# Kernel tuning notes

Hardware: AMD Instinct MI355X
Metric: run time of the kernel (lower is better)

## Reference

```python
import jax, jax.numpy as jnp
import numpy as np

NUM_HEADS = 16
HEAD_DIM = 80
DIM = NUM_HEADS * HEAD_DIM
SEQ = 2048
SCALE = HEAD_DIM ** -0.5


def rotate_half(x):
    x1, x2 = jnp.split(x, 2, axis=-1)
    return jnp.concatenate((-x2, x1), axis=-1)


def setup_inputs() -> dict:
    key = jax.random.key(0)
    ks = jax.random.split(key, 8)
    hidden_states = jax.random.normal(ks[0], (SEQ, DIM), dtype=jnp.float32)
    cu_seqlens = jnp.array([0, SEQ], dtype=jnp.int32)  # unused by the math
    # rotary embeddings for head_dim
    inv_freq = 1.0 / (10000.0 ** (jnp.arange(0, HEAD_DIM // 2, dtype=jnp.float32) / (HEAD_DIM // 2)))
    freqs = jnp.outer(jnp.arange(SEQ, dtype=jnp.float32), inv_freq)  # [S, hd/2]
    emb = jnp.concatenate((freqs, freqs), axis=-1)  # [S, hd]
    cos = jnp.cos(emb)
    sin = jnp.sin(emb)
    w_qkv = jax.random.normal(ks[1], (3 * DIM, DIM), dtype=jnp.float32) * (DIM ** -0.5)
    b_qkv = jax.random.normal(ks[2], (3 * DIM,), dtype=jnp.float32) * 0.02
    w_proj = jax.random.normal(ks[3], (DIM, DIM), dtype=jnp.float32) * (DIM ** -0.5)
    b_proj = jax.random.normal(ks[4], (DIM,), dtype=jnp.float32) * 0.02
    return {"hidden_states": hidden_states, "cu_seqlens": cu_seqlens, "cos": cos,
            "sin": sin, "w_qkv": w_qkv, "b_qkv": b_qkv, "w_proj": w_proj, "b_proj": b_proj}


def reference(hidden_states, cu_seqlens, cos, sin, w_qkv, b_qkv, w_proj, b_proj):
    S = hidden_states.shape[0]
    qkv = hidden_states @ w_qkv.T + b_qkv  # [S, 3*D]
    qkv = qkv.reshape(S, 3, NUM_HEADS, HEAD_DIM)
    q, k, v = qkv[:, 0], qkv[:, 1], qkv[:, 2]  # each [S, H, hd]
    c = cos[:, None, :]  # [S, 1, hd]
    s = sin[:, None, :]
    q = q * c + rotate_half(q) * s
    k = k * c + rotate_half(k) * s
    # SDPA, non-causal: [H, S, S]
    scores = jnp.einsum('shd,thd->hst', q, k) * SCALE
    attn = jax.nn.softmax(scores, axis=-1)
    out = jnp.einsum('hst,thd->shd', attn, v).reshape(S, DIM)
    return out @ w_proj.T + b_proj
```

## Files before the change

### kernel.cpp

```cpp
#include <hip/hip_runtime.h>


#define SEQLEN   2048
#define DIMM     1280
#define NHEADS   16
#define HD       80
#define HDP      96
#define QKV_N    3840
#define NSPLIT   4
#define KVSPAN   (SEQLEN / NSPLIT)
#define QSCALE_LOG2E 0.16130083587064776f

#define KSTRIDE  104
#define VSTRIDE  72
#define PSTRIDE  72

#define EXP2F(x) __builtin_amdgcn_exp2f(x)

#define GLD16(gptr, lptr)                                                      \
    __builtin_amdgcn_global_load_lds(                                          \
        (const __attribute__((address_space(1))) void*)(gptr),                 \
        (__attribute__((address_space(3))) void*)(lptr), 16, 0, 0)

typedef float f32x4 __attribute__((ext_vector_type(4)));
typedef _Float16 half8 __attribute__((ext_vector_type(8)));
typedef _Float16 half4 __attribute__((ext_vector_type(4)));

static __device__ __forceinline__ f32x4 mfma_16x16x32(half8 a, half8 b, f32x4 c) {
    return __builtin_amdgcn_mfma_f32_16x16x32_f16(a, b, c, 0, 0, 0);
}

__global__ void cast_f32_f16(const float* __restrict__ src,
                             _Float16* __restrict__ dst, int n4) {
    int i = blockIdx.x * blockDim.x + threadIdx.x;
    if (i < n4) {
        const float4 v = ((const float4*)src)[i];
        half4 h;
        h.x = (_Float16)v.x; h.y = (_Float16)v.y;
        h.z = (_Float16)v.z; h.w = (_Float16)v.w;
        ((half4*)dst)[i] = h;
    }
}

template<bool OUT_F16>
__global__ __launch_bounds__(256, 2)
void gemm_bt(const _Float16* __restrict__ A, const _Float16* __restrict__ B,
             const float* __restrict__ bias, void* __restrict__ Cout,
             int M, int N, int K) {
    __shared__ __align__(16) _Float16 As[128 * 32];
    __shared__ __align__(16) _Float16 Bs[128 * 32];
    const int tid  = threadIdx.x;
    const int lane = tid & 63;
    const int wave = tid >> 6;
    const int l15  = lane & 15;
    const int quad = lane >> 4;
    const int wm   = wave & 1;
    const int wn   = wave >> 1;
    const long bm = blockIdx.x, bn = blockIdx.y;

    const _Float16* Ag = A + bm * 128 * (long)K;
    const _Float16* Bg = B + bn * 128 * (long)K;

    const int srow = lane >> 2;
    const int scol = (lane & 3) * 8;
    f32x4 acc[4][4] = {};

    for (int k0 = 0; k0 < K; k0 += 32) {
        __syncthreads();
#pragma unroll
        for (int cc = 0; cc < 2; cc++) {
            const int c = wave + cc * 4;
            const long row = 16 * c + srow;
            GLD16(Ag + row * K + k0 + scol, As + 512 * c + lane * 8);
            GLD16(Bg + row * K + k0 + scol, Bs + 512 * c + lane * 8);
        }
        __syncthreads();
        half8 af[4], bf[4];
#pragma unroll
        for (int t = 0; t < 4; t++) {
            af[t] = *(const half8*)&As[(wm * 64 + t * 16 + l15) * 32 + quad * 8];
            bf[t] = *(const half8*)&Bs[(wn * 64 + t * 16 + l15) * 32 + quad * 8];
        }
#pragma unroll
        for (int mt = 0; mt < 4; mt++)
#pragma unroll
            for (int nt = 0; nt < 4; nt++)
                acc[mt][nt] = mfma_16x16x32(af[mt], bf[nt], acc[mt][nt]);
    }

    float bv[4];
#pragma unroll
    for (int nt = 0; nt < 4; nt++)
        bv[nt] = bias[bn * 128 + wn * 64 + nt * 16 + l15];

#pragma unroll
    for (int mt = 0; mt < 4; mt++) {
#pragma unroll
        for (int r = 0; r < 4; r++) {
            const long row = bm * 128 + wm * 64 + mt * 16 + quad * 4 + r;
#pragma unroll
            for (int nt = 0; nt < 4; nt++) {
                const long col = bn * 128 + wn * 64 + nt * 16 + l15;
                const float v = acc[mt][nt][r] + bv[nt];
                if (OUT_F16) ((_Float16*)Cout)[row * (long)N + col] = (_Float16)v;
                else         ((float*)Cout)[row * (long)N + col] = v;
            }
        }
    }
}

__global__ void rope_repack(const _Float16* __restrict__ qkv,
                            const float* __restrict__ cosb,
                            const float* __restrict__ sinb,
                            _Float16* __restrict__ Qh,
                            _Float16* __restrict__ Kh,
                            _Float16* __restrict__ Vh) {
    const int s = blockIdx.x;
    const int tid = threadIdx.x;
    const _Float16* row = qkv + (long)s * QKV_N;

    for (int i = tid; i < NHEADS * 40; i += 256) {
        const int h = i / 40, d = i - h * 40;
        const float c  = cosb[s * HD + d];
        const float sn = sinb[s * HD + d];
        const long o = ((long)h * SEQLEN + s) * HDP;
        const float q0 = (float)row[h * HD + d];
        const float q1 = (float)row[h * HD + d + 40];
        Qh[o + d]      = (_Float16)((q0 * c - q1 * sn) * QSCALE_LOG2E);
        Qh[o + d + 40] = (_Float16)((q1 * c + q0 * sn) * QSCALE_LOG2E);
        const float k0 = (float)row[DIMM + h * HD + d];
        const float k1 = (float)row[DIMM + h * HD + d + 40];
        Kh[o + d]      = (_Float16)(k0 * c - k1 * sn);
        Kh[o + d + 40] = (_Float16)(k1 * c + k0 * sn);
    }
    for (int i = tid; i < NHEADS * HD; i += 256) {
        const int h = i / HD, d = i - h * HD;
        Vh[((long)h * SEQLEN + s) * HDP + d] = row[2 * DIMM + i];
    }
    for (int i = tid; i < NHEADS * 16; i += 256) {
        const int h = i >> 4, d = HD + (i & 15);
        const long o = ((long)h * SEQLEN + s) * HDP + d;
        Qh[o] = (_Float16)0.f; Kh[o] = (_Float16)0.f;
    }
}

__global__ __launch_bounds__(256)
void v_transpose(const _Float16* __restrict__ Vh, _Float16* __restrict__ Vt) {
    const int s0 = blockIdx.x * 64;
    const int h  = blockIdx.y;
    __shared__ __align__(16) _Float16 Ts[64 * 88];
    const int tid = threadIdx.x;
    for (int i = tid; i < 640; i += 256) {
        const int r = i / 10, c = (i - r * 10) * 8;
        *(half8*)&Ts[r * 88 + c] =
            *(const half8*)&Vh[((long)h * SEQLEN + s0 + r) * HDP + c];
    }
    __syncthreads();
    for (int i = tid; i < 640; i += 256) {
        const int d = i >> 3, sc = (i & 7) * 8;
        half8 v;
#pragma unroll
        for (int j = 0; j < 8; j++) v[j] = Ts[(sc + j) * 88 + d];
        *(half8*)&Vt[((long)h * HD + d) * SEQLEN + s0 + sc] = v;
    }
}

__global__ __launch_bounds__(512, 6)
void attn_kernel(const _Float16* __restrict__ Qh, const _Float16* __restrict__ Kh,
                 const _Float16* __restrict__ Vt,
                 _Float16* __restrict__ Ohat0, _Float16* __restrict__ Ohat1,
                 float* __restrict__ Lpart) {
    const int s0 = blockIdx.x * 128;
    const int h  = blockIdx.y;
    const int z  = blockIdx.z;
    __shared__ __align__(16) _Float16 Ks[64 * KSTRIDE];
    __shared__ __align__(16) _Float16 Vts[HD * VSTRIDE];
    __shared__ __align__(16) _Float16 Ps[8][16 * PSTRIDE];

    const int tid  = threadIdx.x;
    const int lane = tid & 63;
    const int wave = tid >> 6;
    const int l15  = lane & 15;
    const int quad = lane >> 4;

    const _Float16* Qg = Qh + ((long)h * SEQLEN + s0 + wave * 16 + l15) * HDP;
    half8 qf[3];
#pragma unroll
    for (int kk = 0; kk < 3; kk++)
        qf[kk] = *(const half8*)&Qg[kk * 32 + quad * 8];

    f32x4 oacc[5] = {};
    float l_r[4] = {0.f, 0.f, 0.f, 0.f};

    for (int t0 = z * KVSPAN; t0 < (z + 1) * KVSPAN; t0 += 64) {
        __syncthreads();
        const _Float16* Kg = Kh + ((long)h * SEQLEN + t0) * HDP;
        for (int i = tid; i < 768; i += 512) {
            const int r = i / 12, c = (i - r * 12) * 8;
            *(half8*)&Ks[r * KSTRIDE + c] = *(const half8*)&Kg[(long)r * HDP + c];
        }
        const _Float16* Vtg = Vt + (long)h * HD * SEQLEN + t0;
        for (int i = tid; i < 640; i += 512) {
            const int d = i >> 3, c = (i & 7) * 8;
            *(half8*)&Vts[d * VSTRIDE + c] = *(const half8*)&Vtg[(long)d * SEQLEN + c];
        }
        __syncthreads();

        f32x4 sa[4] = {};
#pragma unroll
        for (int kk = 0; kk < 3; kk++)
#pragma unroll
            for (int ct = 0; ct < 4; ct++) {
                half8 b = *(const half8*)&Ks[(ct * 16 + l15) * KSTRIDE + kk * 32 + quad * 8];
                sa[ct] = mfma_16x16x32(qf[kk], b, sa[ct]);
            }

        float p[4][4];
#pragma unroll
        for (int ct = 0; ct < 4; ct++)
#pragma unroll
            for (int r = 0; r < 4; r++) {
                p[ct][r] = EXP2F(sa[ct][r]);
                l_r[r] += p[ct][r];
                Ps[wave][(quad * 4 + r) * PSTRIDE + ct * 16 + l15] = (_Float16)p[ct][r];
            }
        asm volatile("s_waitcnt lgkmcnt(0)" ::: "memory");
        half8 pf0 = *(const half8*)&Ps[wave][l15 * PSTRIDE + quad * 8];
        half8 pf1 = *(const half8*)&Ps[wave][l15 * PSTRIDE + 32 + quad * 8];
#pragma unroll
        for (int nt = 0; nt < 5; nt++) {
            half8 v0 = *(const half8*)&Vts[(nt * 16 + l15) * VSTRIDE + quad * 8];
            half8 v1 = *(const half8*)&Vts[(nt * 16 + l15) * VSTRIDE + 32 + quad * 8];
            oacc[nt] = mfma_16x16x32(pf0, v0, oacc[nt]);
            oacc[nt] = mfma_16x16x32(pf1, v1, oacc[nt]);
        }
    }

#pragma unroll
    for (int off = 1; off < 16; off <<= 1)
#pragma unroll
        for (int r = 0; r < 4; r++)
            l_r[r] += __shfl_xor(l_r[r], off);

    float inv[4];
#pragma unroll
    for (int r = 0; r < 4; r++) inv[r] = 1.0f / l_r[r];

    _Float16* Oz = (z < 2) ? Ohat0 : Ohat1;
    const long obase = ((long)(z & 1) * NHEADS + h) * SEQLEN;
    const long lbase = ((long)z * NHEADS + h) * SEQLEN;
#pragma unroll
    for (int nt = 0; nt < 5; nt++)
#pragma unroll
        for (int r = 0; r < 4; r++) {
            const long row = s0 + wave * 16 + quad * 4 + r;
            Oz[(obase + row) * HD + nt * 16 + l15] = (_Float16)(oacc[nt][r] * inv[r]);
        }
    if (l15 == 0)
#pragma unroll
        for (int r = 0; r < 4; r++)
            Lpart[lbase + s0 + wave * 16 + quad * 4 + r] = l_r[r];
}

__global__ __launch_bounds__(256)
void attn_combine(const _Float16* __restrict__ Ohat0,
                  const _Float16* __restrict__ Ohat1,
                  const float* __restrict__ Lp,
                  _Float16* __restrict__ attnb) {
    const int i = blockIdx.x * 256 + threadIdx.x;
    if (i >= SEQLEN * DIMM / 4) return;
    const int flat = i * 4;
    const int s = flat / DIMM;
    const int rem = flat - s * DIMM;
    const int h = rem / HD;
    const int d = rem - h * HD;
    float l[NSPLIT], lsum = 0.f;
#pragma unroll
    for (int zi = 0; zi < NSPLIT; zi++) {
        l[zi] = Lp[((long)zi * NHEADS + h) * SEQLEN + s];
        lsum += l[zi];
    }
    const float invl = 1.0f / lsum;
    float acc[4] = {0.f, 0.f, 0.f, 0.f};
#pragma unroll
    for (int zi = 0; zi < NSPLIT; zi++) {
        const _Float16* Oz = (zi < 2) ? Ohat0 : Ohat1;
        const long obase = ((long)(zi & 1) * NHEADS + h) * SEQLEN;
        const half4 o = *(const half4*)&Oz[(obase + s) * HD + d];
        const float w = l[zi] * invl;
#pragma unroll
        for (int j = 0; j < 4; j++) acc[j] += (float)o[j] * w;
    }
    half4 o;
#pragma unroll
    for (int j = 0; j < 4; j++) o[j] = (_Float16)acc[j];
    *(half4*)&attnb[(long)s * DIMM + rem] = o;
}

extern "C" void kernel_launch(void* const* d_in, const int* in_sizes, int n_in,
                              void* d_out, int out_size, void* d_ws, size_t ws_size,
                              hipStream_t stream) {
    const float* hs     = (const float*)d_in[0];
    const float* cosb   = (const float*)d_in[2];
    const float* sinb   = (const float*)d_in[3];
    const float* w_qkv  = (const float*)d_in[4];
    const float* b_qkv  = (const float*)d_in[5];
    const float* w_proj = (const float*)d_in[6];
    const float* b_proj = (const float*)d_in[7];
    float* out = (float*)d_out;

    _Float16* hsb    = (_Float16*)d_ws;
    _Float16* wqkvb  = hsb    + (long)SEQLEN * DIMM;
    _Float16* wprojb = wqkvb  + (long)QKV_N * DIMM;
    _Float16* qkv    = wprojb + (long)DIMM * DIMM;
    _Float16* Qh     = qkv    + (long)SEQLEN * QKV_N;
    _Float16* Kh     = Qh     + (long)NHEADS * SEQLEN * HDP;
    _Float16* Vh     = Kh     + (long)NHEADS * SEQLEN * HDP;
    _Float16* Vtb    = Vh     + (long)NHEADS * SEQLEN * HDP;
    _Float16* attnb  = Vtb    + (long)NHEADS * HD * SEQLEN;

    _Float16* Ohat0  = (_Float16*)d_ws;
    float*    LpartB = (float*)(Ohat0 + (long)2 * NHEADS * SEQLEN * HD);
    _Float16* Ohat1  = qkv;

    {
        int n4 = SEQLEN * DIMM / 4;
        cast_f32_f16<<<(n4 + 255) / 256, 256, 0, stream>>>(hs, hsb, n4);
        n4 = QKV_N * DIMM / 4;
        cast_f32_f16<<<(n4 + 255) / 256, 256, 0, stream>>>(w_qkv, wqkvb, n4);
        n4 = DIMM * DIMM / 4;
        cast_f32_f16<<<(n4 + 255) / 256, 256, 0, stream>>>(w_proj, wprojb, n4);
    }

    gemm_bt<true><<<dim3(SEQLEN / 128, QKV_N / 128), 256, 0, stream>>>(
        hsb, wqkvb, b_qkv, qkv, SEQLEN, QKV_N, DIMM);

    rope_repack<<<SEQLEN, 256, 0, stream>>>(qkv, cosb, sinb, Qh, Kh, Vh);

    v_transpose<<<dim3(SEQLEN / 64, NHEADS), 256, 0, stream>>>(Vh, Vtb);

    attn_kernel<<<dim3(SEQLEN / 128, NHEADS, NSPLIT), 512, 0, stream>>>(
        Qh, Kh, Vtb, Ohat0, Ohat1, LpartB);

    attn_combine<<<(SEQLEN * DIMM / 4 + 255) / 256, 256, 0, stream>>>(
        Ohat0, Ohat1, LpartB, attnb);

    gemm_bt<false><<<dim3(SEQLEN / 128, DIMM / 128), 256, 0, stream>>>(
        attnb, wprojb, b_proj, out, SEQLEN, DIMM, DIMM);
}
```

Before: 228.9 us.

## Keep attention P in registers via transposed MFMA, vectorize RoPE, merge casts

```diff
diff --git a/kernel.cpp b/kernel.cpp
--- a/kernel.cpp
+++ b/kernel.cpp
@@ -13,7 +13,6 @@
 
 #define KSTRIDE  104
 #define VSTRIDE  72
-#define PSTRIDE  72
 
 #define EXP2F(x) __builtin_amdgcn_exp2f(x)
 
@@ -29,17 +28,26 @@
 static __device__ __forceinline__ f32x4 mfma_16x16x32(half8 a, half8 b, f32x4 c) {
     return __builtin_amdgcn_mfma_f32_16x16x32_f16(a, b, c, 0, 0, 0);
 }
-
-__global__ void cast_f32_f16(const float* __restrict__ src,
-                             _Float16* __restrict__ dst, int n4) {
-    int i = blockIdx.x * blockDim.x + threadIdx.x;
-    if (i < n4) {
-        const float4 v = ((const float4*)src)[i];
-        half4 h;
-        h.x = (_Float16)v.x; h.y = (_Float16)v.y;
-        h.z = (_Float16)v.z; h.w = (_Float16)v.w;
-        ((half4*)dst)[i] = h;
-    }
+static __device__ __forceinline__ f32x4 mfma_16x16x16(half4 a, half4 b, f32x4 c) {
+    return __builtin_amdgcn_mfma_f32_16x16x16f16(a, b, c, 0, 0, 0);
+}
+
+__global__ __launch_bounds__(256)
+void cast_all(const float* __restrict__ hs, const float* __restrict__ wq,
+              const float* __restrict__ wp, _Float16* __restrict__ dhs,
+              _Float16* __restrict__ dwq, _Float16* __restrict__ dwp) {
+    const int n1 = SEQLEN * DIMM / 4, n2 = QKV_N * DIMM / 4, n3 = DIMM * DIMM / 4;
+    int i = blockIdx.x * 256 + threadIdx.x;
+    const float4* src; half4* dst; int j;
+    if (i < n1)           { src = (const float4*)hs; dst = (half4*)dhs; j = i; }
+    else if (i < n1 + n2) { src = (const float4*)wq; dst = (half4*)dwq; j = i - n1; }
+    else if (i < n1 + n2 + n3) { src = (const float4*)wp; dst = (half4*)dwp; j = i - n1 - n2; }
+    else return;
+    const float4 v = src[j];
+    half4 h;
+    h.x = (_Float16)v.x; h.y = (_Float16)v.y;
+    h.z = (_Float16)v.z; h.w = (_Float16)v.w;
+    dst[j] = h;
 }
 
 template<bool OUT_F16>
@@ -109,38 +117,53 @@
     }
 }
 
-__global__ void rope_repack(const _Float16* __restrict__ qkv,
-                            const float* __restrict__ cosb,
-                            const float* __restrict__ sinb,
-                            _Float16* __restrict__ Qh,
-                            _Float16* __restrict__ Kh,
-                            _Float16* __restrict__ Vh) {
+__global__ __launch_bounds__(256)
+void rope_repack(const _Float16* __restrict__ qkv,
+                 const float* __restrict__ cosb,
+                 const float* __restrict__ sinb,
+                 _Float16* __restrict__ Qh,
+                 _Float16* __restrict__ Kh,
+                 _Float16* __restrict__ Vh) {
     const int s = blockIdx.x;
     const int tid = threadIdx.x;
     const _Float16* row = qkv + (long)s * QKV_N;
 
-    for (int i = tid; i < NHEADS * 40; i += 256) {
-        const int h = i / 40, d = i - h * 40;
-        const float c  = cosb[s * HD + d];
-        const float sn = sinb[s * HD + d];
+    for (int i = tid; i < NHEADS * 5; i += 256) {
+        const int h = i / 5, d = (i - h * 5) * 8;
+        const half8 q0 = *(const half8*)&row[h * HD + d];
+        const half8 q1 = *(const half8*)&row[h * HD + d + 40];
+        const half8 k0 = *(const half8*)&row[DIMM + h * HD + d];
+        const half8 k1 = *(const half8*)&row[DIMM + h * HD + d + 40];
+        const float4 cA = *(const float4*)&cosb[s * HD + d];
+        const float4 cB = *(const float4*)&cosb[s * HD + d + 4];
+        const float4 sA = *(const float4*)&sinb[s * HD + d];
+        const float4 sB = *(const float4*)&sinb[s * HD + d + 4];
+        half8 qo0, qo1, ko0, ko1;
+#pragma unroll
+        for (int j = 0; j < 8; j++) {
+            const float cj = (j < 4) ? cA[j] : cB[j - 4];
+            const float sj = (j < 4) ? sA[j] : sB[j - 4];
+            qo0[j] = (_Float16)(((float)q0[j] * cj - (float)q1[j] * sj) * QSCALE_LOG2E);
+            qo1[j] = (_Float16)(((float)q1[j] * cj + (float)q0[j] * sj) * QSCALE_LOG2E);
+            ko0[j] = (_Float16)((float)k0[j] * cj - (float)k1[j] * sj);
+            ko1[j] = (_Float16)((float)k1[j] * cj + (float)k0[j] * sj);
+        }
         const long o = ((long)h * SEQLEN + s) * HDP;
-        const float q0 = (float)row[h * HD + d];
-        const float q1 = (float)row[h * HD + d + 40];
-        Qh[o + d]      = (_Float16)((q0 * c - q1 * sn) * QSCALE_LOG2E);
-        Qh[o + d + 40] = (_Float16)((q1 * c + q0 * sn) * QSCALE_LOG2E);
-        const float k0 = (float)row[DIMM + h * HD + d];
-        const float k1 = (float)row[DIMM + h * HD + d + 40];
-        Kh[o + d]      = (_Float16)(k0 * c - k1 * sn);
-        Kh[o + d + 40] = (_Float16)(k1 * c + k0 * sn);
-    }
-    for (int i = tid; i < NHEADS * HD; i += 256) {
-        const int h = i / HD, d = i - h * HD;
-        Vh[((long)h * SEQLEN + s) * HDP + d] = row[2 * DIMM + i];
-    }
-    for (int i = tid; i < NHEADS * 16; i += 256) {
-        const int h = i >> 4, d = HD + (i & 15);
+        *(half8*)&Qh[o + d]      = qo0;
+        *(half8*)&Qh[o + d + 40] = qo1;
+        *(half8*)&Kh[o + d]      = ko0;
+        *(half8*)&Kh[o + d + 40] = ko1;
+    }
+    for (int i = tid; i < NHEADS * 10; i += 256) {
+        const int h = i / 10, d = (i - h * 10) * 8;
+        *(half8*)&Vh[((long)h * SEQLEN + s) * HDP + d] =
+            *(const half8*)&row[2 * DIMM + h * HD + d];
+    }
+    for (int i = tid; i < NHEADS * 2; i += 256) {
+        const int h = i >> 1, d = HD + (i & 1) * 8;
         const long o = ((long)h * SEQLEN + s) * HDP + d;
-        Qh[o] = (_Float16)0.f; Kh[o] = (_Float16)0.f;
+        *(half8*)&Qh[o] = (half8)(_Float16)0.f;
+        *(half8*)&Kh[o] = (half8)(_Float16)0.f;
     }
 }
 
@@ -165,7 +188,7 @@
     }
 }
 
-__global__ __launch_bounds__(512, 6)
+__global__ __launch_bounds__(512, 8)
 void attn_kernel(const _Float16* __restrict__ Qh, const _Float16* __restrict__ Kh,
                  const _Float16* __restrict__ Vt,
                  _Float16* __restrict__ Ohat0, _Float16* __restrict__ Ohat1,
@@ -175,7 +198,6 @@
     const int z  = blockIdx.z;
     __shared__ __align__(16) _Float16 Ks[64 * KSTRIDE];
     __shared__ __align__(16) _Float16 Vts[HD * VSTRIDE];
-    __shared__ __align__(16) _Float16 Ps[8][16 * PSTRIDE];
 
     const int tid  = threadIdx.x;
     const int lane = tid & 63;
@@ -189,8 +211,8 @@
     for (int kk = 0; kk < 3; kk++)
         qf[kk] = *(const half8*)&Qg[kk * 32 + quad * 8];
 
-    f32x4 oacc[5] = {};
-    float l_r[4] = {0.f, 0.f, 0.f, 0.f};
+    f32x4 oaccT[5] = {};
+    float l_acc = 0.f;
 
     for (int t0 = z * KVSPAN; t0 < (z + 1) * KVSPAN; t0 += 64) {
         __syncthreads();
@@ -211,55 +233,46 @@
         for (int kk = 0; kk < 3; kk++)
 #pragma unroll
             for (int ct = 0; ct < 4; ct++) {
-                half8 b = *(const half8*)&Ks[(ct * 16 + l15) * KSTRIDE + kk * 32 + quad * 8];
-                sa[ct] = mfma_16x16x32(qf[kk], b, sa[ct]);
+                half8 kf = *(const half8*)&Ks[(ct * 16 + l15) * KSTRIDE + kk * 32 + quad * 8];
+                sa[ct] = mfma_16x16x32(kf, qf[kk], sa[ct]);
             }
 
-        float p[4][4];
+        half4 pb[4];
 #pragma unroll
         for (int ct = 0; ct < 4; ct++)
 #pragma unroll
             for (int r = 0; r < 4; r++) {
-                p[ct][r] = EXP2F(sa[ct][r]);
-                l_r[r] += p[ct][r];
-                Ps[wave][(quad * 4 + r) * PSTRIDE + ct * 16 + l15] = (_Float16)p[ct][r];
+                const float p = EXP2F(sa[ct][r]);
+                l_acc += p;
+                pb[ct][r] = (_Float16)p;
             }
-        asm volatile("s_waitcnt lgkmcnt(0)" ::: "memory");
-        half8 pf0 = *(const half8*)&Ps[wave][l15 * PSTRIDE + quad * 8];
-        half8 pf1 = *(const half8*)&Ps[wave][l15 * PSTRIDE + 32 + quad * 8];
-#pragma unroll
-        for (int nt = 0; nt < 5; nt++) {
-            half8 v0 = *(const half8*)&Vts[(nt * 16 + l15) * VSTRIDE + quad * 8];
-            half8 v1 = *(const half8*)&Vts[(nt * 16 + l15) * VSTRIDE + 32 + quad * 8];
-            oacc[nt] = mfma_16x16x32(pf0, v0, oacc[nt]);
-            oacc[nt] = mfma_16x16x32(pf1, v1, oacc[nt]);
-        }
-    }
-
-#pragma unroll
-    for (int off = 1; off < 16; off <<= 1)
-#pragma unroll
-        for (int r = 0; r < 4; r++)
-            l_r[r] += __shfl_xor(l_r[r], off);
-
-    float inv[4];
-#pragma unroll
-    for (int r = 0; r < 4; r++) inv[r] = 1.0f / l_r[r];
+
+#pragma unroll
+        for (int nt = 0; nt < 5; nt++)
+#pragma unroll
+            for (int ct = 0; ct < 4; ct++) {
+                half4 vf = *(const half4*)&Vts[(nt * 16 + l15) * VSTRIDE + ct * 16 + quad * 4];
+                oaccT[nt] = mfma_16x16x16(vf, pb[ct], oaccT[nt]);
+            }
+    }
+
+    l_acc += __shfl_xor(l_acc, 16);
+    l_acc += __shfl_xor(l_acc, 32);
+    const float inv = 1.0f / l_acc;
 
     _Float16* Oz = (z < 2) ? Ohat0 : Ohat1;
     const long obase = ((long)(z & 1) * NHEADS + h) * SEQLEN;
     const long lbase = ((long)z * NHEADS + h) * SEQLEN;
-#pragma unroll
-    for (int nt = 0; nt < 5; nt++)
-#pragma unroll
-        for (int r = 0; r < 4; r++) {
-            const long row = s0 + wave * 16 + quad * 4 + r;
-            Oz[(obase + row) * HD + nt * 16 + l15] = (_Float16)(oacc[nt][r] * inv[r]);
-        }
-    if (l15 == 0)
-#pragma unroll
-        for (int r = 0; r < 4; r++)
-            Lpart[lbase + s0 + wave * 16 + quad * 4 + r] = l_r[r];
+    const long row = s0 + wave * 16 + l15;
+#pragma unroll
+    for (int nt = 0; nt < 5; nt++) {
+        half4 o;
+#pragma unroll
+        for (int r = 0; r < 4; r++) o[r] = (_Float16)(oaccT[nt][r] * inv);
+        *(half4*)&Oz[(obase + row) * HD + nt * 16 + quad * 4] = o;
+    }
+    if (quad == 0)
+        Lpart[lbase + row] = l_acc;
 }
 
 __global__ __launch_bounds__(256)
@@ -324,12 +337,9 @@
     _Float16* Ohat1  = qkv;
 
     {
-        int n4 = SEQLEN * DIMM / 4;
-        cast_f32_f16<<<(n4 + 255) / 256, 256, 0, stream>>>(hs, hsb, n4);
-        n4 = QKV_N * DIMM / 4;
-        cast_f32_f16<<<(n4 + 255) / 256, 256, 0, stream>>>(w_qkv, wqkvb, n4);
-        n4 = DIMM * DIMM / 4;
-        cast_f32_f16<<<(n4 + 255) / 256, 256, 0, stream>>>(w_proj, wprojb, n4);
+        const int ntot = (SEQLEN * DIMM + QKV_N * DIMM + DIMM * DIMM) / 4;
+        cast_all<<<(ntot + 255) / 256, 256, 0, stream>>>(
+            hs, w_qkv, w_proj, hsb, wqkvb, wprojb);
     }
 
     gemm_bt<true><<<dim3(SEQLEN / 128, QKV_N / 128), 256, 0, stream>>>(
```

New measurement: 219.2 us. -4.2%, faster.
